# Performance work log

Measured on AMD Instinct MI355X. Metric: run time of the kernel, lower is better.

Reference implementation:

```python
import jax, jax.numpy as jnp
import numpy as np
import math

HIDDEN = 2048
NUM_HEADS = 16
HEAD_SIZE = HIDDEN // NUM_HEADS
BATCH = 2
SEQ = 2048


def setup_inputs() -> dict:
    key = jax.random.key(0)
    k_x, k_wq, k_bq, k_wo, k_bo = jax.random.split(key, 5)
    scale_in = 1.0 / math.sqrt(HIDDEN)
    return {
        "x": jax.random.normal(k_x, (BATCH, SEQ, HIDDEN), dtype=jnp.float32),
        # torch Linear stored as W[out,in]; we keep the jax-friendly transpose [in,out]
        "Wqkv": jax.random.normal(k_wq, (HIDDEN, 3 * HIDDEN), dtype=jnp.float32) * scale_in,
        "bqkv": jax.random.normal(k_bq, (3 * HIDDEN,), dtype=jnp.float32) * 0.01,
        "Wo": jax.random.normal(k_wo, (HIDDEN, HIDDEN), dtype=jnp.float32) * scale_in,
        "bo": jax.random.normal(k_bo, (HIDDEN,), dtype=jnp.float32) * 0.01,
    }


def reference(x, Wqkv, bqkv, Wo, bo):
    b, s, _ = x.shape
    # fused QKV projection; channel layout is (three, num_heads, head_size)
    kqv = x @ Wqkv + bqkv                      # [b, s, 3*hidden]
    kqv = kqv.reshape(b, s, 3, NUM_HEADS, HEAD_SIZE)
    q = kqv[:, :, 0]                           # [b, s, n, h]
    k = kqv[:, :, 1]
    v = kqv[:, :, 2]
    # scores[b, n, s_key, t_query] = K_s . Q_t, scaled
    scores = jnp.einsum('bsnh,btnh->bnst', k, q) / math.sqrt(HEAD_SIZE)
    # faithful to original: keep upper triangle (key <= query), masked entries are exactly -10000
    ones = jnp.ones_like(scores)
    scores = jnp.triu(scores) + (-10000.0) * jnp.tril(ones, k=-1)
    attn = jax.nn.softmax(scores, axis=2)      # softmax over key dim
    out = jnp.einsum('bnkq,bknh->bqnh', attn, v)  # [b, s, n, h]
    out = out.reshape(b, s, NUM_HEADS * HEAD_SIZE)
    return out @ Wo + bo
```

## Files before the change

kernel.cpp:

```cpp
#include <hip/hip_runtime.h>
#include <hip/hip_bf16.h>

typedef __hip_bfloat16 bf16;
typedef __attribute__((ext_vector_type(8))) short short8;
typedef __attribute__((ext_vector_type(8))) unsigned short ushort8;
typedef __attribute__((ext_vector_type(4))) float floatx4;

#define BATCH 2
#define S_LEN 2048
#define NHEAD 16
#define HD 128
#define HIDDEN 2048
#define QSCALE 0.12754435f

static __device__ __forceinline__ unsigned short f2bf(float f) {
    union { float f; unsigned int u; } c; c.f = f;
    unsigned int u = c.u;
    unsigned int rounded = u + 0x7FFF + ((u >> 16) & 1);
    return (unsigned short)(rounded >> 16);
}

__global__ __launch_bounds__(256) void cast_f32_bf16(const float* __restrict__ src,
                                                     bf16* __restrict__ dst) {
    int i = (blockIdx.x * 256 + threadIdx.x) * 8;
    float4 a = *(const float4*)&src[i];
    float4 b = *(const float4*)&src[i + 4];
    ushort8 o;
    o[0] = f2bf(a.x); o[1] = f2bf(a.y); o[2] = f2bf(a.z); o[3] = f2bf(a.w);
    o[4] = f2bf(b.x); o[5] = f2bf(b.y); o[6] = f2bf(b.z); o[7] = f2bf(b.w);
    *(ushort8*)&dst[i] = o;
}

__global__ __launch_bounds__(256) void cast_transpose(const float* __restrict__ src,
                                                      bf16* __restrict__ dst,
                                                      int R, int C) {
    __shared__ unsigned short t[32][33];
    int tx = threadIdx.x & 31, ty = threadIdx.x >> 5;
    int c0 = blockIdx.x * 32, r0 = blockIdx.y * 32;
#pragma unroll
    for (int i = 0; i < 4; i++) {
        int r = r0 + ty + i * 8;
        t[ty + i * 8][tx] = f2bf(src[(size_t)r * C + c0 + tx]);
    }
    __syncthreads();
#pragma unroll
    for (int i = 0; i < 4; i++) {
        int cc = c0 + ty + i * 8;
        ((unsigned short*)dst)[(size_t)cc * R + r0 + tx] = t[tx][ty + i * 8];
    }
}

__global__ __launch_bounds__(256) void gemm_bt(const bf16* __restrict__ A,
                                               const bf16* __restrict__ Bt,
                                               const float* __restrict__ bias,
                                               bf16* __restrict__ Qb,
                                               bf16* __restrict__ Kb,
                                               bf16* __restrict__ Vt,
                                               int K) {
    __shared__ __align__(16) bf16 As[128 * 32];
    __shared__ __align__(16) bf16 Bs[128 * 32];

    int tid = threadIdx.x;
    int wave = tid >> 6, lane = tid & 63;
    int quad = lane >> 4, lr = lane & 15;
    int wm = wave >> 1, wn = wave & 1;
    int m0 = blockIdx.y * 128, n0 = blockIdx.x * 128;

    const floatx4 fzero = {0.f, 0.f, 0.f, 0.f};
    floatx4 acc[4][4];
#pragma unroll
    for (int i = 0; i < 4; i++)
#pragma unroll
        for (int j = 0; j < 4; j++) acc[i][j] = fzero;

    int rsub = lane >> 2;
    int csub = (lane & 3) * 8;
    const bf16* gA0 = A + (size_t)(m0 + wave * 32 + rsub) * K + csub;
    const bf16* gA1 = gA0 + (size_t)16 * K;
    const bf16* gB0 = Bt + (size_t)(n0 + wave * 32 + rsub) * K + csub;
    const bf16* gB1 = gB0 + (size_t)16 * K;
    bf16* lA0 = As + wave * 1024;
    bf16* lA1 = As + wave * 1024 + 512;
    bf16* lB0 = Bs + wave * 1024;
    bf16* lB1 = Bs + wave * 1024 + 512;

    for (int kt = 0; kt < K; kt += 32) {
        __builtin_amdgcn_global_load_lds(
            (const __attribute__((address_space(1))) void*)(gA0 + kt),
            (__attribute__((address_space(3))) void*)lA0, 16, 0, 0);
        __builtin_amdgcn_global_load_lds(
            (const __attribute__((address_space(1))) void*)(gA1 + kt),
            (__attribute__((address_space(3))) void*)lA1, 16, 0, 0);
        __builtin_amdgcn_global_load_lds(
            (const __attribute__((address_space(1))) void*)(gB0 + kt),
            (__attribute__((address_space(3))) void*)lB0, 16, 0, 0);
        __builtin_amdgcn_global_load_lds(
            (const __attribute__((address_space(1))) void*)(gB1 + kt),
            (__attribute__((address_space(3))) void*)lB1, 16, 0, 0);
        __syncthreads();

        short8 aF[4], bF[4];
#pragma unroll
        for (int i = 0; i < 4; i++)
            aF[i] = *(const short8*)(As + (wm * 64 + i * 16 + lr) * 32 + quad * 8);
#pragma unroll
        for (int j = 0; j < 4; j++)
            bF[j] = *(const short8*)(Bs + (wn * 64 + j * 16 + lr) * 32 + quad * 8);
#pragma unroll
        for (int i = 0; i < 4; i++)
#pragma unroll
            for (int j = 0; j < 4; j++)
                acc[i][j] = __builtin_amdgcn_mfma_f32_16x16x32_bf16(aF[i], bF[j], acc[i][j], 0, 0, 0);
        __syncthreads();
    }

#pragma unroll
    for (int i = 0; i < 4; i++) {
#pragma unroll
        for (int j = 0; j < 4; j++) {
            int gcn = n0 + wn * 64 + j * 16 + lr;
            float bv = bias[gcn];
#pragma unroll
            for (int reg = 0; reg < 4; reg++) {
                int gm = m0 + wm * 64 + i * 16 + quad * 4 + reg;
                float v = acc[i][j][reg] + bv;
                int t = gcn >> 11, hh = (gcn >> 7) & 15, d = gcn & 127;
                int bb = gm >> 11, s = gm & 2047;
                size_t hb = (size_t)(bb * NHEAD + hh);
                if (t == 0) {
                    Qb[(hb * S_LEN + s) * HD + d] = __float2bfloat16(v * QSCALE);
                } else if (t == 1) {
                    Kb[(hb * S_LEN + s) * HD + d] = __float2bfloat16(v);
                } else {
                    Vt[(hb * HD + d) * S_LEN + s] = __float2bfloat16(v);
                }
            }
        }
    }
}

__global__ __launch_bounds__(256) void gemm_out(const bf16* __restrict__ A,
                                                const bf16* __restrict__ Bt,
                                                const float* __restrict__ bias,
                                                float* __restrict__ C,
                                                int N, int K) {
    __shared__ __align__(16) bf16 As[128 * 32];
    __shared__ __align__(16) bf16 Bs[128 * 32];

    int tid = threadIdx.x;
    int wave = tid >> 6, lane = tid & 63;
    int quad = lane >> 4, lr = lane & 15;
    int wm = wave >> 1, wn = wave & 1;
    int m0 = blockIdx.y * 128, n0 = blockIdx.x * 128;

    const floatx4 fzero = {0.f, 0.f, 0.f, 0.f};
    floatx4 acc[4][4];
#pragma unroll
    for (int i = 0; i < 4; i++)
#pragma unroll
        for (int j = 0; j < 4; j++) acc[i][j] = fzero;

    int rsub = lane >> 2;
    int csub = (lane & 3) * 8;
    const bf16* gA0 = A + (size_t)(m0 + wave * 32 + rsub) * K + csub;
    const bf16* gA1 = gA0 + (size_t)16 * K;
    const bf16* gB0 = Bt + (size_t)(n0 + wave * 32 + rsub) * K + csub;
    const bf16* gB1 = gB0 + (size_t)16 * K;
    bf16* lA0 = As + wave * 1024;
    bf16* lA1 = As + wave * 1024 + 512;
    bf16* lB0 = Bs + wave * 1024;
    bf16* lB1 = Bs + wave * 1024 + 512;

    for (int kt = 0; kt < K; kt += 32) {
        __builtin_amdgcn_global_load_lds(
            (const __attribute__((address_space(1))) void*)(gA0 + kt),
            (__attribute__((address_space(3))) void*)lA0, 16, 0, 0);
        __builtin_amdgcn_global_load_lds(
            (const __attribute__((address_space(1))) void*)(gA1 + kt),
            (__attribute__((address_space(3))) void*)lA1, 16, 0, 0);
        __builtin_amdgcn_global_load_lds(
            (const __attribute__((address_space(1))) void*)(gB0 + kt),
            (__attribute__((address_space(3))) void*)lB0, 16, 0, 0);
        __builtin_amdgcn_global_load_lds(
            (const __attribute__((address_space(1))) void*)(gB1 + kt),
            (__attribute__((address_space(3))) void*)lB1, 16, 0, 0);
        __syncthreads();

        short8 aF[4], bF[4];
#pragma unroll
        for (int i = 0; i < 4; i++)
            aF[i] = *(const short8*)(As + (wm * 64 + i * 16 + lr) * 32 + quad * 8);
#pragma unroll
        for (int j = 0; j < 4; j++)
            bF[j] = *(const short8*)(Bs + (wn * 64 + j * 16 + lr) * 32 + quad * 8);
#pragma unroll
        for (int i = 0; i < 4; i++)
#pragma unroll
            for (int j = 0; j < 4; j++)
                acc[i][j] = __builtin_amdgcn_mfma_f32_16x16x32_bf16(aF[i], bF[j], acc[i][j], 0, 0, 0);
        __syncthreads();
    }

#pragma unroll
    for (int i = 0; i < 4; i++) {
#pragma unroll
        for (int j = 0; j < 4; j++) {
            int gcn = n0 + wn * 64 + j * 16 + lr;
            float bv = bias[gcn];
#pragma unroll
            for (int reg = 0; reg < 4; reg++) {
                int gm = m0 + wm * 64 + i * 16 + quad * 4 + reg;
                C[(size_t)gm * N + gcn] = acc[i][j][reg] + bv;
            }
        }
    }
}

#define PSTR 72
__global__ __launch_bounds__(256, 2) void attn_kernel(const bf16* __restrict__ Qb,
                                                      const bf16* __restrict__ Kb,
                                                      const bf16* __restrict__ Vt,
                                                      bf16* __restrict__ Obuf) {
    __shared__ __align__(16) bf16 Ks[64 * 128];
    __shared__ __align__(16) bf16 Vs[128 * 64];
    __shared__ __align__(16) bf16 Ps[4][32 * PSTR];

    int tid = threadIdx.x;
    int wave = tid >> 6, lane = tid & 63;
    int quad = lane >> 4, lr = lane & 15;
    int srow = lane >> 4;
    int head = blockIdx.x, p = blockIdx.y, b = blockIdx.z;
    size_t hb = (size_t)(b * NHEAD + head);
    const bf16* Qbase = Qb + hb * S_LEN * HD;
    const bf16* Kbase = Kb + hb * S_LEN * HD;
    const bf16* Vbase = Vt + hb * (size_t)HD * S_LEN;

    const floatx4 fzero = {0.f, 0.f, 0.f, 0.f};
    const float MASKV = -30000.f;

    for (int sub = 0; sub < 2; sub++) {
        int qt = sub ? (15 - p) : p;
        int q0 = qt * 128;
        int niter = 2 * qt + 2;

        short8 qF[2][4];
#pragma unroll
        for (int mt = 0; mt < 2; mt++)
#pragma unroll
            for (int kc = 0; kc < 4; kc++)
                qF[mt][kc] = *(const short8*)&Qbase[(size_t)(q0 + wave * 32 + mt * 16 + lr) * HD + kc * 32 + quad * 8];

        floatx4 Oacc[2][8];
        float mrow[2][4], lrow[2][4];
#pragma unroll
        for (int mt = 0; mt < 2; mt++) {
#pragma unroll
            for (int dn = 0; dn < 8; dn++) Oacc[mt][dn] = fzero;
#pragma unroll
            for (int r = 0; r < 4; r++) { mrow[mt][r] = -30000.f; lrow[mt][r] = 0.f; }
        }

        for (int kt = 0; kt < niter; kt++) {
            int ks0 = kt * 64;
            __syncthreads();
#pragma unroll
            for (int i = 0; i < 4; i++) {
                int rl = wave * 16 + i * 4 + srow;
                int gc = lr ^ (rl & 15);
                __builtin_amdgcn_global_load_lds(
                    (const __attribute__((address_space(1))) void*)(Kbase + (size_t)(ks0 + rl) * HD + gc * 8),
                    (__attribute__((address_space(3))) void*)(Ks + (wave * 16 + i * 4) * 128), 16, 0, 0);
            }
#pragma unroll
            for (int i = 0; i < 4; i++) {
                int vr = wave * 32 + i * 8 + (lane >> 3);
                int gvc = (lane & 7) ^ (vr & 7);
                __builtin_amdgcn_global_load_lds(
                    (const __attribute__((address_space(1))) void*)(Vbase + (size_t)vr * S_LEN + ks0 + gvc * 8),
                    (__attribute__((address_space(3))) void*)(Vs + (wave * 32 + i * 8) * 64), 16, 0, 0);
            }
            __syncthreads();

            floatx4 sc[2][4];
#pragma unroll
            for (int mt = 0; mt < 2; mt++)
#pragma unroll
                for (int nt = 0; nt < 4; nt++) sc[mt][nt] = fzero;
#pragma unroll
            for (int kc = 0; kc < 4; kc++)
#pragma unroll
                for (int nt = 0; nt < 4; nt++) {
                    short8 kf = *(const short8*)&Ks[(nt * 16 + lr) * 128 + (((kc * 4 + quad) ^ lr) & 15) * 8];
#pragma unroll
                    for (int mt = 0; mt < 2; mt++)
                        sc[mt][nt] = __builtin_amdgcn_mfma_f32_16x16x32_bf16(qF[mt][kc], kf, sc[mt][nt], 0, 0, 0);
                }
            if (kt >= 2 * qt) {
                int koff = (kt - 2 * qt) * 64;
#pragma unroll
                for (int mt = 0; mt < 2; mt++)
#pragma unroll
                    for (int nt = 0; nt < 4; nt++)
#pragma unroll
                        for (int reg = 0; reg < 4; reg++) {
                            int qg = wave * 32 + mt * 16 + quad * 4 + reg;
                            int kg = koff + nt * 16 + lr;
                            if (kg > qg) sc[mt][nt][reg] = MASKV;
                        }
            }
#pragma unroll
            for (int mt = 0; mt < 2; mt++) {
                float pm[4], alpha[4], rs[4];
#pragma unroll
                for (int r = 0; r < 4; r++) {
                    pm[r] = sc[mt][0][r];
#pragma unroll
                    for (int nt = 1; nt < 4; nt++) pm[r] = fmaxf(pm[r], sc[mt][nt][r]);
                }
#pragma unroll
                for (int off = 1; off < 16; off <<= 1)
#pragma unroll
                    for (int r = 0; r < 4; r++) pm[r] = fmaxf(pm[r], __shfl_xor(pm[r], off, 64));
#pragma unroll
                for (int r = 0; r < 4; r++) {
                    float mn = fmaxf(mrow[mt][r], pm[r]);
                    alpha[r] = __builtin_amdgcn_exp2f(mrow[mt][r] - mn);
                    mrow[mt][r] = mn;
                    rs[r] = 0.f;
                }
#pragma unroll
                for (int nt = 0; nt < 4; nt++)
#pragma unroll
                    for (int r = 0; r < 4; r++) {
                        float pv = __builtin_amdgcn_exp2f(sc[mt][nt][r] - mrow[mt][r]);
                        rs[r] += pv;
                        Ps[wave][(mt * 16 + quad * 4 + r) * PSTR + nt * 16 + lr] = __float2bfloat16(pv);
                    }
#pragma unroll
                for (int off = 1; off < 16; off <<= 1)
#pragma unroll
                    for (int r = 0; r < 4; r++) rs[r] += __shfl_xor(rs[r], off, 64);
#pragma unroll
                for (int r = 0; r < 4; r++) lrow[mt][r] = lrow[mt][r] * alpha[r] + rs[r];
#pragma unroll
                for (int dn = 0; dn < 8; dn++)
#pragma unroll
                    for (int r = 0; r < 4; r++) Oacc[mt][dn][r] *= alpha[r];
            }
#pragma unroll
            for (int st = 0; st < 2; st++) {
                short8 aP[2];
#pragma unroll
                for (int mt = 0; mt < 2; mt++)
                    aP[mt] = *(const short8*)&Ps[wave][(mt * 16 + lr) * PSTR + st * 32 + quad * 8];
#pragma unroll
                for (int dn = 0; dn < 8; dn++) {
                    short8 vf = *(const short8*)&Vs[(dn * 16 + lr) * 64 + (((st * 4 + quad) ^ (lr & 7)) & 7) * 8];
#pragma unroll
                    for (int mt = 0; mt < 2; mt++)
                        Oacc[mt][dn] = __builtin_amdgcn_mfma_f32_16x16x32_bf16(aP[mt], vf, Oacc[mt][dn], 0, 0, 0);
                }
            }
        }

#pragma unroll
        for (int mt = 0; mt < 2; mt++)
#pragma unroll
            for (int reg = 0; reg < 4; reg++) {
                float inv = 1.0f / lrow[mt][reg];
                int qg = q0 + wave * 32 + mt * 16 + quad * 4 + reg;
#pragma unroll
                for (int dn = 0; dn < 8; dn++) {
                    int d = dn * 16 + lr;
                    Obuf[((size_t)(b * S_LEN + qg)) * HIDDEN + head * HD + d] =
                        __float2bfloat16(Oacc[mt][dn][reg] * inv);
                }
            }
    }
}

extern "C" void kernel_launch(void* const* d_in, const int* in_sizes, int n_in,
                              void* d_out, int out_size, void* d_ws, size_t ws_size,
                              hipStream_t stream) {
    (void)in_sizes; (void)n_in; (void)out_size; (void)ws_size;
    const float* x    = (const float*)d_in[0];
    const float* Wqkv = (const float*)d_in[1];
    const float* bqkv = (const float*)d_in[2];
    const float* Wo   = (const float*)d_in[3];
    const float* bo   = (const float*)d_in[4];
    float* out = (float*)d_out;

    bf16* ws = (bf16*)d_ws;
    bf16* Xb    = ws;
    bf16* Obuf  = ws;
    bf16* WqkvT = ws + (size_t)8388608;
    bf16* WoT   = WqkvT;
    bf16* Qb    = WqkvT + (size_t)12582912;
    bf16* Kb    = Qb + (size_t)8388608;
    bf16* Vt    = Kb + (size_t)8388608;

    cast_f32_bf16<<<4096, 256, 0, stream>>>(x, Xb);
    cast_transpose<<<dim3(192, 64), 256, 0, stream>>>(Wqkv, WqkvT, 2048, 6144);
    gemm_bt<<<dim3(48, 32), 256, 0, stream>>>(Xb, WqkvT, bqkv, Qb, Kb, Vt, 2048);
    cast_transpose<<<dim3(64, 64), 256, 0, stream>>>(Wo, WoT, 2048, 2048);
    attn_kernel<<<dim3(16, 8, 2), 256, 0, stream>>>(Qb, Kb, Vt, Obuf);
    gemm_out<<<dim3(16, 32), 256, 0, stream>>>(Obuf, WoT, bo, out, 2048, 2048);
}
```

Measured before the change: 445.6 us.

## Shrink attention query tile to 64 rows and double grid size

Result: no change. 441.8 us (-0.9%).

```diff
diff --git a/kernel.cpp b/kernel.cpp
--- a/kernel.cpp
+++ b/kernel.cpp
@@ -223,7 +223,7 @@
                                                       bf16* __restrict__ Obuf) {
     __shared__ __align__(16) bf16 Ks[64 * 128];
     __shared__ __align__(16) bf16 Vs[128 * 64];
-    __shared__ __align__(16) bf16 Ps[4][32 * PSTR];
+    __shared__ __align__(16) bf16 Ps[4][16 * PSTR];
 
     int tid = threadIdx.x;
     int wave = tid >> 6, lane = tid & 63;
@@ -239,26 +239,21 @@
     const float MASKV = -30000.f;
 
     for (int sub = 0; sub < 2; sub++) {
-        int qt = sub ? (15 - p) : p;
-        int q0 = qt * 128;
-        int niter = 2 * qt + 2;
-
-        short8 qF[2][4];
-#pragma unroll
-        for (int mt = 0; mt < 2; mt++)
-#pragma unroll
-            for (int kc = 0; kc < 4; kc++)
-                qF[mt][kc] = *(const short8*)&Qbase[(size_t)(q0 + wave * 32 + mt * 16 + lr) * HD + kc * 32 + quad * 8];
-
-        floatx4 Oacc[2][8];
-        float mrow[2][4], lrow[2][4];
-#pragma unroll
-        for (int mt = 0; mt < 2; mt++) {
-#pragma unroll
-            for (int dn = 0; dn < 8; dn++) Oacc[mt][dn] = fzero;
-#pragma unroll
-            for (int r = 0; r < 4; r++) { mrow[mt][r] = -30000.f; lrow[mt][r] = 0.f; }
-        }
+        int qt = sub ? (31 - p) : p;
+        int q0 = qt * 64;
+        int niter = qt + 1;
+
+        short8 qF[4];
+#pragma unroll
+        for (int kc = 0; kc < 4; kc++)
+            qF[kc] = *(const short8*)&Qbase[(size_t)(q0 + wave * 16 + lr) * HD + kc * 32 + quad * 8];
+
+        floatx4 Oacc[8];
+        float mrow[4], lrow[4];
+#pragma unroll
+        for (int dn = 0; dn < 8; dn++) Oacc[dn] = fzero;
+#pragma unroll
+        for (int r = 0; r < 4; r++) { mrow[r] = -30000.f; lrow[r] = 0.f; }
 
         for (int kt = 0; kt < niter; kt++) {
             int ks0 = kt * 64;
@@ -281,41 +276,33 @@
             }
             __syncthreads();
 
-            floatx4 sc[2][4];
-#pragma unroll
-            for (int mt = 0; mt < 2; mt++)
-#pragma unroll
-                for (int nt = 0; nt < 4; nt++) sc[mt][nt] = fzero;
+            floatx4 sc[4];
+#pragma unroll
+            for (int nt = 0; nt < 4; nt++) sc[nt] = fzero;
 #pragma unroll
             for (int kc = 0; kc < 4; kc++)
 #pragma unroll
                 for (int nt = 0; nt < 4; nt++) {
                     short8 kf = *(const short8*)&Ks[(nt * 16 + lr) * 128 + (((kc * 4 + quad) ^ lr) & 15) * 8];
-#pragma unroll
-                    for (int mt = 0; mt < 2; mt++)
-                        sc[mt][nt] = __builtin_amdgcn_mfma_f32_16x16x32_bf16(qF[mt][kc], kf, sc[mt][nt], 0, 0, 0);
-                }
-            if (kt >= 2 * qt) {
-                int koff = (kt - 2 * qt) * 64;
-#pragma unroll
-                for (int mt = 0; mt < 2; mt++)
-#pragma unroll
-                    for (int nt = 0; nt < 4; nt++)
-#pragma unroll
-                        for (int reg = 0; reg < 4; reg++) {
-                            int qg = wave * 32 + mt * 16 + quad * 4 + reg;
-                            int kg = koff + nt * 16 + lr;
-                            if (kg > qg) sc[mt][nt][reg] = MASKV;
-                        }
-            }
-#pragma unroll
-            for (int mt = 0; mt < 2; mt++) {
+                    sc[nt] = __builtin_amdgcn_mfma_f32_16x16x32_bf16(qF[kc], kf, sc[nt], 0, 0, 0);
+                }
+            if (kt == niter - 1) {
+#pragma unroll
+                for (int nt = 0; nt < 4; nt++)
+#pragma unroll
+                    for (int reg = 0; reg < 4; reg++) {
+                        int qg = wave * 16 + quad * 4 + reg;
+                        int kg = nt * 16 + lr;
+                        if (kg > qg) sc[nt][reg] = MASKV;
+                    }
+            }
+            {
                 float pm[4], alpha[4], rs[4];
 #pragma unroll
                 for (int r = 0; r < 4; r++) {
-                    pm[r] = sc[mt][0][r];
-#pragma unroll
-                    for (int nt = 1; nt < 4; nt++) pm[r] = fmaxf(pm[r], sc[mt][nt][r]);
+                    pm[r] = sc[0][r];
+#pragma unroll
+                    for (int nt = 1; nt < 4; nt++) pm[r] = fmaxf(pm[r], sc[nt][r]);
                 }
 #pragma unroll
                 for (int off = 1; off < 16; off <<= 1)
@@ -323,59 +310,52 @@
                     for (int r = 0; r < 4; r++) pm[r] = fmaxf(pm[r], __shfl_xor(pm[r], off, 64));
 #pragma unroll
                 for (int r = 0; r < 4; r++) {
-                    float mn = fmaxf(mrow[mt][r], pm[r]);
-                    alpha[r] = __builtin_amdgcn_exp2f(mrow[mt][r] - mn);
-                    mrow[mt][r] = mn;
+                    float mn = fmaxf(mrow[r], pm[r]);
+                    alpha[r] = __builtin_amdgcn_exp2f(mrow[r] - mn);
+                    mrow[r] = mn;
                     rs[r] = 0.f;
                 }
 #pragma unroll
                 for (int nt = 0; nt < 4; nt++)
 #pragma unroll
                     for (int r = 0; r < 4; r++) {
-                        float pv = __builtin_amdgcn_exp2f(sc[mt][nt][r] - mrow[mt][r]);
+                        float pv = __builtin_amdgcn_exp2f(sc[nt][r] - mrow[r]);
                         rs[r] += pv;
-                        Ps[wave][(mt * 16 + quad * 4 + r) * PSTR + nt * 16 + lr] = __float2bfloat16(pv);
+                        Ps[wave][(quad * 4 + r) * PSTR + nt * 16 + lr] = __float2bfloat16(pv);
                     }
 #pragma unroll
                 for (int off = 1; off < 16; off <<= 1)
 #pragma unroll
                     for (int r = 0; r < 4; r++) rs[r] += __shfl_xor(rs[r], off, 64);
 #pragma unroll
-                for (int r = 0; r < 4; r++) lrow[mt][r] = lrow[mt][r] * alpha[r] + rs[r];
+                for (int r = 0; r < 4; r++) lrow[r] = lrow[r] * alpha[r] + rs[r];
 #pragma unroll
                 for (int dn = 0; dn < 8; dn++)
 #pragma unroll
-                    for (int r = 0; r < 4; r++) Oacc[mt][dn][r] *= alpha[r];
+                    for (int r = 0; r < 4; r++) Oacc[dn][r] *= alpha[r];
             }
 #pragma unroll
             for (int st = 0; st < 2; st++) {
-                short8 aP[2];
-#pragma unroll
-                for (int mt = 0; mt < 2; mt++)
-                    aP[mt] = *(const short8*)&Ps[wave][(mt * 16 + lr) * PSTR + st * 32 + quad * 8];
+                short8 aP = *(const short8*)&Ps[wave][lr * PSTR + st * 32 + quad * 8];
 #pragma unroll
                 for (int dn = 0; dn < 8; dn++) {
                     short8 vf = *(const short8*)&Vs[(dn * 16 + lr) * 64 + (((st * 4 + quad) ^ (lr & 7)) & 7) * 8];
-#pragma unroll
-                    for (int mt = 0; mt < 2; mt++)
-                        Oacc[mt][dn] = __builtin_amdgcn_mfma_f32_16x16x32_bf16(aP[mt], vf, Oacc[mt][dn], 0, 0, 0);
+                    Oacc[dn] = __builtin_amdgcn_mfma_f32_16x16x32_bf16(aP, vf, Oacc[dn], 0, 0, 0);
                 }
             }
         }
 
 #pragma unroll
-        for (int mt = 0; mt < 2; mt++)
-#pragma unroll
-            for (int reg = 0; reg < 4; reg++) {
-                float inv = 1.0f / lrow[mt][reg];
-                int qg = q0 + wave * 32 + mt * 16 + quad * 4 + reg;
-#pragma unroll
-                for (int dn = 0; dn < 8; dn++) {
-                    int d = dn * 16 + lr;
-                    Obuf[((size_t)(b * S_LEN + qg)) * HIDDEN + head * HD + d] =
-                        __float2bfloat16(Oacc[mt][dn][reg] * inv);
-                }
-            }
+        for (int reg = 0; reg < 4; reg++) {
+            float inv = 1.0f / lrow[reg];
+            int qg = q0 + wave * 16 + quad * 4 + reg;
+#pragma unroll
+            for (int dn = 0; dn < 8; dn++) {
+                int d = dn * 16 + lr;
+                Obuf[((size_t)(b * S_LEN + qg)) * HIDDEN + head * HD + d] =
+                    __float2bfloat16(Oacc[dn][reg] * inv);
+            }
+        }
     }
 }
 
@@ -403,6 +383,6 @@
     cast_transpose<<<dim3(192, 64), 256, 0, stream>>>(Wqkv, WqkvT, 2048, 6144);
     gemm_bt<<<dim3(48, 32), 256, 0, stream>>>(Xb, WqkvT, bqkv, Qb, Kb, Vt, 2048);
     cast_transpose<<<dim3(64, 64), 256, 0, stream>>>(Wo, WoT, 2048, 2048);
-    attn_kernel<<<dim3(16, 8, 2), 256, 0, stream>>>(Qb, Kb, Vt, Obuf);
+    attn_kernel<<<dim3(16, 16, 2), 256, 0, stream>>>(Qb, Kb, Vt, Obuf);
     gemm_out<<<dim3(16, 32), 256, 0, stream>>>(Obuf, WoT, bo, out, 2048, 2048);
 }
```
